# Kernel tuning notes

Hardware: AMD Instinct MI355X
Metric: run time of the kernel (lower is better)

Reference implementation:

```python
import jax, jax.numpy as jnp
import numpy as np

B, T, D = 32, 256, 384
MAX_LEN = 2048

def setup_inputs() -> dict:
    key = jax.random.key(0)
    k1, k2 = jax.random.split(key)
    x = jax.random.normal(k1, (B, T, D), dtype=jnp.float32)
    duration = jax.random.randint(k2, (B, T), 0, 8, dtype=jnp.int64)
    return {"x": x, "duration": duration, "max_len": MAX_LEN}


def reference(x, duration, max_len):
    # x: [B, T, D] phoneme features; duration: [B, T] int repeat counts.
    # Fused expand-by-duration + pad via cumulative offsets + gather.
    csum = jnp.cumsum(duration, axis=1)                       # [B, T]
    mel_len = csum[:, -1]                                     # [B]
    frames = jnp.arange(max_len)                              # [max_len]
    # frame j belongs to phoneme i where csum[i-1] <= j < csum[i]
    idx = jax.vmap(lambda c: jnp.searchsorted(c, frames, side='right'))(csum)  # [B, max_len]
    valid = frames[None, :] < mel_len[:, None]                # [B, max_len]
    idx = jnp.clip(idx, 0, x.shape[1] - 1)
    out = jnp.take_along_axis(x, idx[:, :, None], axis=1)     # [B, max_len, D]
    out = jnp.where(valid[:, :, None], out, 0.0)
    return out, mel_len
```

## Files before the change

kernel.cpp:

```cpp
#include <hip/hip_runtime.h>


#define BB 32
#define TT 256
#define DD 384
#define MAXLEN 2048
#define D4 (DD / 4)
#define FPB 8
#define TILES (MAXLEN / FPB)

__global__ __launch_bounds__(256) void scan_kernel(const int* __restrict__ duration,
                                                   int* __restrict__ csum,
                                                   float* __restrict__ mel_out) {
    __shared__ int s[TT];
    const int b = blockIdx.x;
    const int t = threadIdx.x;
    s[t] = duration[b * TT + t];
    __syncthreads();
    for (int off = 1; off < TT; off <<= 1) {
        int cur = s[t];
        int add = (t >= off) ? s[t - off] : 0;
        __syncthreads();
        s[t] = cur + add;
        __syncthreads();
    }
    csum[b * TT + t] = s[t];
    if (t == TT - 1) {
        mel_out[b] = (float)s[t];
    }
}

__global__ __launch_bounds__(256) void expand_kernel(const float* __restrict__ x,
                                                     const int* __restrict__ csum,
                                                     float* __restrict__ out) {
    __shared__ int s_csum[TT];
    __shared__ int s_idx[FPB];

    const int bid = blockIdx.x;
    const int b = bid >> 8;
    const int tile = bid & (TILES - 1);
    const int tid = threadIdx.x;

    s_csum[tid] = csum[b * TT + tid];
    __syncthreads();

    if (tid < FPB) {
        const int f = tile * FPB + tid;
        const int mel = s_csum[TT - 1];
        int idx = -1;
        if (f < mel) {
            int lo = 0, hi = TT;
            while (lo < hi) {
                int mid = (lo + hi) >> 1;
                if (s_csum[mid] > f) hi = mid; else lo = mid + 1;
            }
            idx = lo;
        }
        s_idx[tid] = idx;
    }
    __syncthreads();

    const float4* __restrict__ x4 = (const float4*)(x + (size_t)b * TT * DD);
    float4* __restrict__ o4 = (float4*)(out + ((size_t)b * MAXLEN + (size_t)tile * FPB) * DD);

    #pragma unroll
    for (int i = 0; i < (FPB * D4) / 256; ++i) {
        const int g = i * 256 + tid;
        const int fl = g / D4;
        const int vv = g - fl * D4;
        const int idx = s_idx[fl];
        float4 val;
        if (idx >= 0) {
            val = x4[idx * D4 + vv];
        } else {
            val = make_float4(0.f, 0.f, 0.f, 0.f);
        }
        o4[g] = val;
    }
}

extern "C" void kernel_launch(void* const* d_in, const int* in_sizes, int n_in,
                              void* d_out, int out_size, void* d_ws, size_t ws_size,
                              hipStream_t stream) {
    const float* x = (const float*)d_in[0];
    const int* duration = (const int*)d_in[1];

    float* out = (float*)d_out;
    float* mel_out = out + (size_t)BB * MAXLEN * DD;
    int* csum = (int*)d_ws;

    scan_kernel<<<BB, TT, 0, stream>>>(duration, csum, mel_out);
    expand_kernel<<<BB * TILES, 256, 0, stream>>>(x, csum, out);
}
```

Measured before the change: 121.0 us.

## Fuse duration scan into expand kernel with wave-shuffle scan and nontemporal stores

Removes the separate scan kernel and its csum round trip through global memory. Each expand block now recomputes the prefix sum of its batch row with wave shuffles plus a small cross-wave combine, and fills frame indices by scatter from each phoneme instead of binary search. Frames per block are doubled to halve the redundant scans, and output writes use nontemporal stores. The cost is recomputing the scan in every block and running fewer, larger blocks.

Measured after the change: 124.6 us. 1.03x slower.

```diff
diff --git a/kernel.cpp b/kernel.cpp
--- a/kernel.cpp
+++ b/kernel.cpp
@@ -6,62 +6,57 @@
 #define DD 384
 #define MAXLEN 2048
 #define D4 (DD / 4)
-#define FPB 8
+#define FPB 16
 #define TILES (MAXLEN / FPB)
 
-__global__ __launch_bounds__(256) void scan_kernel(const int* __restrict__ duration,
-                                                   int* __restrict__ csum,
-                                                   float* __restrict__ mel_out) {
-    __shared__ int s[TT];
-    const int b = blockIdx.x;
-    const int t = threadIdx.x;
-    s[t] = duration[b * TT + t];
-    __syncthreads();
-    for (int off = 1; off < TT; off <<= 1) {
-        int cur = s[t];
-        int add = (t >= off) ? s[t - off] : 0;
-        __syncthreads();
-        s[t] = cur + add;
-        __syncthreads();
-    }
-    csum[b * TT + t] = s[t];
-    if (t == TT - 1) {
-        mel_out[b] = (float)s[t];
-    }
-}
+typedef float v4f __attribute__((ext_vector_type(4)));
 
-__global__ __launch_bounds__(256) void expand_kernel(const float* __restrict__ x,
-                                                     const int* __restrict__ csum,
-                                                     float* __restrict__ out) {
+__global__ __launch_bounds__(256) void lr_fused(const float* __restrict__ x,
+                                                const int* __restrict__ duration,
+                                                float* __restrict__ out,
+                                                float* __restrict__ mel_out) {
     __shared__ int s_csum[TT];
+    __shared__ int s_wsum[4];
     __shared__ int s_idx[FPB];
 
     const int bid = blockIdx.x;
-    const int b = bid >> 8;
+    const int b = bid >> 7;
     const int tile = bid & (TILES - 1);
     const int tid = threadIdx.x;
+    const int lane = tid & 63;
+    const int wave = tid >> 6;
 
-    s_csum[tid] = csum[b * TT + tid];
+    const int d = duration[b * TT + tid];
+    int v = d;
+    #pragma unroll
+    for (int off = 1; off < 64; off <<= 1) {
+        int n = __shfl_up(v, off, 64);
+        if (lane >= off) v += n;
+    }
+    if (lane == 63) s_wsum[wave] = v;
+    if (tid < FPB) s_idx[tid] = -1;
+    __syncthreads();
+    int prefix = 0;
+    #pragma unroll
+    for (int w = 0; w < 4; ++w) prefix += (w < wave) ? s_wsum[w] : 0;
+    const int cend = v + prefix;
+    s_csum[tid] = cend;
     __syncthreads();
 
-    if (tid < FPB) {
-        const int f = tile * FPB + tid;
-        const int mel = s_csum[TT - 1];
-        int idx = -1;
-        if (f < mel) {
-            int lo = 0, hi = TT;
-            while (lo < hi) {
-                int mid = (lo + hi) >> 1;
-                if (s_csum[mid] > f) hi = mid; else lo = mid + 1;
-            }
-            idx = lo;
-        }
-        s_idx[tid] = idx;
+    const int mel = s_csum[TT - 1];
+    if (tile == 0 && tid == 0) mel_out[b] = (float)mel;
+
+    const int base = tile * FPB;
+    {
+        const int cstart = cend - d;
+        int lo = cstart > base ? cstart : base;
+        int hi = cend < base + FPB ? cend : base + FPB;
+        for (int f = lo; f < hi; ++f) s_idx[f - base] = tid;
     }
     __syncthreads();
 
-    const float4* __restrict__ x4 = (const float4*)(x + (size_t)b * TT * DD);
-    float4* __restrict__ o4 = (float4*)(out + ((size_t)b * MAXLEN + (size_t)tile * FPB) * DD);
+    const v4f* __restrict__ x4 = (const v4f*)(x + (size_t)b * TT * DD);
+    v4f* __restrict__ o4 = (v4f*)(out + ((size_t)b * MAXLEN + base) * DD);
 
     #pragma unroll
     for (int i = 0; i < (FPB * D4) / 256; ++i) {
@@ -69,13 +64,9 @@
         const int fl = g / D4;
         const int vv = g - fl * D4;
         const int idx = s_idx[fl];
-        float4 val;
-        if (idx >= 0) {
-            val = x4[idx * D4 + vv];
-        } else {
-            val = make_float4(0.f, 0.f, 0.f, 0.f);
-        }
-        o4[g] = val;
+        v4f val = (v4f)(0.f);
+        if (idx >= 0) val = x4[idx * D4 + vv];
+        __builtin_nontemporal_store(val, &o4[g]);
     }
 }
 
@@ -87,8 +78,6 @@
 
     float* out = (float*)d_out;
     float* mel_out = out + (size_t)BB * MAXLEN * DD;
-    int* csum = (int*)d_ws;
 
-    scan_kernel<<<BB, TT, 0, stream>>>(duration, csum, mel_out);
-    expand_kernel<<<BB * TILES, 256, 0, stream>>>(x, csum, out);
+    lr_fused<<<BB * TILES, 256, 0, stream>>>(x, duration, out, mel_out);
 }
```
